# Performance work log

Hardware: AMD Instinct MI355X
Metric: run time of the kernel (lower is better)

The kernel has to match this reference:

```python
import jax, jax.numpy as jnp
import numpy as np

N_AGENTS, OBS_DIM, HID, ACT_DIM = 8192, 64, 128, 16


def setup_inputs() -> dict:
    key = jax.random.key(0)
    k = jax.random.split(key, 8)
    obs_agents = jax.random.normal(k[0], (N_AGENTS, OBS_DIM), dtype=jnp.float32)
    # binary adjacency, {0,1}, int32 (index/mask semantics, non-differentiable)
    adj = jax.random.randint(k[1], (N_AGENTS, N_AGENTS), 0, 2, dtype=jnp.int32)
    def lin(kk, fan_in, fan_out):
        lim = 1.0 / np.sqrt(fan_in)
        kw, kb = jax.random.split(kk)
        W = jax.random.uniform(kw, (fan_in, fan_out), jnp.float32, -lim, lim)
        b = jax.random.uniform(kb, (fan_out,), jnp.float32, -lim, lim)
        return W, b
    W1, b1 = lin(k[2], OBS_DIM, HID)          # encoder
    W2, b2 = lin(k[3], 2 * HID, HID)          # actor layer 1
    W3, b3 = lin(k[4], HID, ACT_DIM)          # actor layer 2
    return {"obs_agents": obs_agents, "adj": adj,
            "W1": W1, "b1": b1, "W2": W2, "b2": b2, "W3": W3, "b3": b3}


def reference(obs_agents, adj, W1, b1, W2, b2, W3, b3):
    # per-agent encode: h = tanh(obs @ W1 + b1)  -> [N, HID]
    h = jnp.tanh(obs_agents @ W1 + b1)
    # neighbor mean message: mean of h[j] over j with adj[i,j]!=0, zeros if no neighbors
    a = adj.astype(h.dtype)                      # [N, N] binary
    deg = jnp.sum(a, axis=1, keepdims=True)      # [N, 1]
    msg = (a @ h) / jnp.maximum(deg, 1.0)        # zero rows stay zero
    # actor MLP on concat([h, msg])
    combined = jnp.concatenate([h, msg], axis=-1)            # [N, 2*HID]
    hid = jnp.tanh(combined @ W2 + b2)                        # [N, HID]
    logits = hid @ W3 + b3                                    # [N, ACT_DIM]
    return logits
```

## Files before the change

kernel.cpp:

```cpp
#include <hip/hip_runtime.h>
#include <stdint.h>
#include <math.h>

#define NAG 8192
#define NB  144
#define BM  64
#define BK  32
#define NSPLIT 8

typedef __attribute__((ext_vector_type(8))) short short8;
typedef __attribute__((ext_vector_type(4))) float floatx4;

__device__ __forceinline__ float bf2f(unsigned short u) {
    union { uint32_t i; float f; } v; v.i = ((uint32_t)u) << 16; return v.f;
}
__device__ __forceinline__ unsigned short f2bf(float f) {
    union { float f; uint32_t i; } v; v.f = f;
    uint32_t x = v.i;
    return (unsigned short)((x + 0x7FFFu + ((x >> 16) & 1u)) >> 16);
}
__device__ __forceinline__ unsigned short f2h(float f) {
    union { _Float16 h; unsigned short u; } v; v.h = (_Float16)f; return v.u;
}
__device__ __forceinline__ float h2f(unsigned short u) {
    union { _Float16 h; unsigned short u; } v; v.u = u; return (float)v.h;
}
__device__ __forceinline__ void gload_lds16(const void* g, void* lds) {
    __builtin_amdgcn_global_load_lds(
        (const __attribute__((address_space(1))) uint32_t*)g,
        (__attribute__((address_space(3))) uint32_t*)lds, 16, 0, 0);
}

__global__ __launch_bounds__(64) void k0_init(
    int* __restrict__ flag, const unsigned short* __restrict__ W1raw)
{
    int big = 0;
    #pragma unroll
    for (int j = 0; j < 8; ++j) {
        float v = bf2f(W1raw[threadIdx.x * 8 + j]);
        if (!(fabsf(v) <= 1e6f)) big = 1;
    }
    unsigned long long m = __ballot(big);
    if (threadIdx.x == 0) *flag = (m != 0ull) ? 1 : 0;
}

__global__ __launch_bounds__(256) void k1_encode(
    const void* __restrict__ obs,
    const void* __restrict__ W1,
    const void* __restrict__ b1,
    const int* __restrict__ flag,
    float* __restrict__ h_f32,
    unsigned short* __restrict__ hT)
{
    __shared__ float obs_lds[32][68];
    __shared__ unsigned short ht_lds[128][33];
    const int t = threadIdx.x;
    const int abase = blockIdx.x * 32;
    const bool isf = (*flag != 0);

    {
        int a = t >> 3, c0 = (t & 7) * 8;
        if (isf) {
            const float* p = (const float*)obs;
            #pragma unroll
            for (int j = 0; j < 8; ++j)
                obs_lds[a][c0 + j] = p[(size_t)(abase + a) * 64 + c0 + j];
        } else {
            const unsigned short* p = (const unsigned short*)obs;
            #pragma unroll
            for (int j = 0; j < 8; ++j)
                obs_lds[a][c0 + j] = bf2f(p[(size_t)(abase + a) * 64 + c0 + j]);
        }
    }
    __syncthreads();

    const int o = t & 127;
    const int half = t >> 7;
    float acc[16];
    if (isf) {
        const float* Wp = (const float*)W1;
        float bias = ((const float*)b1)[o];
        #pragma unroll
        for (int i = 0; i < 16; ++i) acc[i] = bias;
        for (int k0 = 0; k0 < 64; k0 += 8) {
            float w[8];
            #pragma unroll
            for (int j = 0; j < 8; ++j) w[j] = Wp[(k0 + j) * 128 + o];
            #pragma unroll
            for (int j = 0; j < 8; ++j)
                #pragma unroll
                for (int i = 0; i < 16; ++i)
                    acc[i] = fmaf(obs_lds[half * 16 + i][k0 + j], w[j], acc[i]);
        }
    } else {
        const unsigned short* Wp = (const unsigned short*)W1;
        float bias = bf2f(((const unsigned short*)b1)[o]);
        #pragma unroll
        for (int i = 0; i < 16; ++i) acc[i] = bias;
        for (int k0 = 0; k0 < 64; k0 += 8) {
            float w[8];
            #pragma unroll
            for (int j = 0; j < 8; ++j) w[j] = bf2f(Wp[(k0 + j) * 128 + o]);
            #pragma unroll
            for (int j = 0; j < 8; ++j)
                #pragma unroll
                for (int i = 0; i < 16; ++i)
                    acc[i] = fmaf(obs_lds[half * 16 + i][k0 + j], w[j], acc[i]);
        }
    }
    #pragma unroll
    for (int i = 0; i < 16; ++i) {
        float th = tanhf(acc[i]);
        int a = half * 16 + i;
        h_f32[(size_t)(abase + a) * 128 + o] = th;
        ht_lds[o][a] = f2bf(th);
    }
    __syncthreads();

    for (int p = 0; p < 18; ++p) {
        int n = p * 8 + (t >> 5);
        int a = t & 31;
        unsigned short v;
        if (n < 128)       v = ht_lds[n][a];
        else if (n == 128) v = 0x3F80;
        else               v = 0;
        hT[(size_t)n * NAG + abase + a] = v;
    }
}

__global__ __launch_bounds__(256, 4) void k2_msggemm(
    const int* __restrict__ adj,
    const unsigned short* __restrict__ hT,
    unsigned short* __restrict__ Cp16)
{
    __shared__ __align__(16) int Alds0[64 * BK];
    __shared__ __align__(16) int Alds1[64 * BK];
    __shared__ __align__(16) unsigned short Blds0[144 * BK];
    __shared__ __align__(16) unsigned short Blds1[144 * BK];
    const int t = threadIdx.x;
    const int mtile = blockIdx.x & 127;
    const int ks = blockIdx.x >> 7;
    const int row0 = mtile * BM;
    const int kbeg = ks * 1024;

    const int wave = t >> 6, lane = t & 63;
    const int fm = lane & 15, quad = lane >> 4;

    floatx4 acc[9];
    #pragma unroll
    for (int i = 0; i < 9; ++i) acc[i] = (floatx4)0.f;

    const int rowA = wave * 8 + (lane >> 3);
    const int cA = (lane & 7) ^ (rowA & 7);
    const int* aS0 = adj + (size_t)(row0 + rowA) * NAG + kbeg + cA * 4;
    const int* aS1 = adj + (size_t)(row0 + rowA + 32) * NAG + kbeg + cA * 4;
    const int rowB = wave * 16 + (lane >> 2);
    const int cB = (lane & 3) ^ ((rowB >> 1) & 3);
    const unsigned short* bS0 = hT + (size_t)rowB * NAG + kbeg + cB * 8;
    const unsigned short* bS1 = hT + (size_t)(rowB + 64) * NAG + kbeg + cB * 8;
    int* Ad00 = Alds0 + wave * 256;  int* Ad01 = Alds0 + 1024 + wave * 256;
    int* Ad10 = Alds1 + wave * 256;  int* Ad11 = Alds1 + 1024 + wave * 256;
    unsigned short* Bd00 = Blds0 + wave * 512;  unsigned short* Bd01 = Blds0 + 2048 + wave * 512;
    unsigned short* Bd10 = Blds1 + wave * 512;  unsigned short* Bd11 = Blds1 + 2048 + wave * 512;

    {
        int rr = 128 + (t >> 4);
        int off = (t & 15) * 2;
        uint32_t vv = (rr == 128) ? 0x3F803F80u : 0u;
        *reinterpret_cast<uint32_t*>(&Blds0[rr * BK + off]) = vv;
        *reinterpret_cast<uint32_t*>(&Blds1[rr * BK + off]) = vv;
    }

#define DMA(T, Ad0_, Ad1_, Bd0_, Bd1_) do { \
        gload_lds16(aS0 + (T) * BK, (Ad0_)); \
        gload_lds16(aS1 + (T) * BK, (Ad1_)); \
        gload_lds16(bS0 + (T) * BK, (Bd0_)); \
        gload_lds16(bS1 + (T) * BK, (Bd1_)); \
    } while (0)
#define COMPUTE(Ab, Bb) do { \
        const int arow = (wave * 16 + fm) * BK; \
        int4 v0 = *reinterpret_cast<const int4*>(&(Ab)[arow + (((quad * 2 + 0) ^ (fm & 7)) << 2)]); \
        int4 v1 = *reinterpret_cast<const int4*>(&(Ab)[arow + (((quad * 2 + 1) ^ (fm & 7)) << 2)]); \
        union { uint32_t u[4]; short8 s; } af; \
        af.u[0] = ((uint32_t)v0.x | ((uint32_t)v0.y << 16)) * 0x3F80u; \
        af.u[1] = ((uint32_t)v0.z | ((uint32_t)v0.w << 16)) * 0x3F80u; \
        af.u[2] = ((uint32_t)v1.x | ((uint32_t)v1.y << 16)) * 0x3F80u; \
        af.u[3] = ((uint32_t)v1.z | ((uint32_t)v1.w << 16)) * 0x3F80u; \
        const int bphys = (quad ^ ((fm >> 1) & 3)) << 3; \
        _Pragma("unroll") \
        for (int j = 0; j < 9; ++j) { \
            short8 bf = *reinterpret_cast<const short8*>(&(Bb)[(j * 16 + fm) * BK + bphys]); \
            acc[j] = __builtin_amdgcn_mfma_f32_16x16x32_bf16(af.s, bf, acc[j], 0, 0, 0); \
        } \
    } while (0)

    DMA(0, Ad00, Ad01, Bd00, Bd01);

    for (int it = 0; it < 32; it += 2) {
        __syncthreads();
        DMA(it + 1, Ad10, Ad11, Bd10, Bd11);
        COMPUTE(Alds0, Blds0);
        __syncthreads();
        if (it + 2 < 32) DMA(it + 2, Ad00, Ad01, Bd00, Bd01);
        COMPUTE(Alds1, Blds1);
    }

    unsigned short* out = Cp16 + (size_t)ks * (NAG * NB);
    #pragma unroll
    for (int j = 0; j < 9; ++j) {
        int col = j * 16 + fm;
        #pragma unroll
        for (int r = 0; r < 4; ++r) {
            int row = row0 + wave * 16 + quad * 4 + r;
            out[(size_t)row * NB + col] = f2h(acc[j][r]);
        }
    }
#undef DMA
#undef COMPUTE
}

__global__ __launch_bounds__(256) void k3_actor(
    const float* __restrict__ h_f32,
    const unsigned short* __restrict__ Cp16,
    const void* __restrict__ W2,
    const void* __restrict__ b2,
    const void* __restrict__ W3,
    const void* __restrict__ b3,
    const int* __restrict__ flag,
    void* __restrict__ out)
{
    __shared__ float4 comb4[16][66];
    __shared__ float hid[16][132];
    __shared__ float inv_lds[16];
    const int t = threadIdx.x;
    const int abase = blockIdx.x * 16;
    const bool isf = (*flag != 0);
    const size_t PS = (size_t)NAG * NB;

    if (t < 16) {
        float deg = 0.f;
        #pragma unroll
        for (int s = 0; s < NSPLIT; ++s)
            deg += h2f(Cp16[s * PS + (size_t)(abase + t) * NB + 128]);
        inv_lds[t] = 1.0f / fmaxf(deg, 1.0f);
    }
    __syncthreads();

    #pragma unroll
    for (int jj = 0; jj < 4; ++jj) {
        int idx = jj * 256 + t;
        int a = idx >> 6, q = idx & 63;
        float4 v;
        if (q < 32) {
            v = *reinterpret_cast<const float4*>(h_f32 + (size_t)(abase + a) * 128 + q * 4);
        } else {
            int f = (q - 32) * 4;
            float s0 = 0.f, s1 = 0.f, s2 = 0.f, s3 = 0.f;
            #pragma unroll
            for (int s = 0; s < NSPLIT; ++s) {
                ushort4 p = *reinterpret_cast<const ushort4*>(Cp16 + s * PS + (size_t)(abase + a) * NB + f);
                s0 += h2f(p.x); s1 += h2f(p.y); s2 += h2f(p.z); s3 += h2f(p.w);
            }
            float sc = inv_lds[a];
            v = make_float4(s0 * sc, s1 * sc, s2 * sc, s3 * sc);
        }
        comb4[a][q] = v;
    }
    __syncthreads();

    const int o = t & 127, half = t >> 7;
    float acc[8];
    if (isf) {
        const float* Wp = (const float*)W2;
        float bias = ((const float*)b2)[o];
        #pragma unroll
        for (int i = 0; i < 8; ++i) acc[i] = bias;
        for (int cq = 0; cq < 64; ++cq) {
            float w0 = Wp[(cq * 4 + 0) * 128 + o];
            float w1 = Wp[(cq * 4 + 1) * 128 + o];
            float w2 = Wp[(cq * 4 + 2) * 128 + o];
            float w3 = Wp[(cq * 4 + 3) * 128 + o];
            #pragma unroll
            for (int i = 0; i < 8; ++i) {
                float4 v = comb4[half * 8 + i][cq];
                acc[i] = fmaf(v.x, w0, acc[i]);
                acc[i] = fmaf(v.y, w1, acc[i]);
                acc[i] = fmaf(v.z, w2, acc[i]);
                acc[i] = fmaf(v.w, w3, acc[i]);
            }
        }
    } else {
        const unsigned short* Wp = (const unsigned short*)W2;
        float bias = bf2f(((const unsigned short*)b2)[o]);
        #pragma unroll
        for (int i = 0; i < 8; ++i) acc[i] = bias;
        for (int cq = 0; cq < 64; ++cq) {
            float w0 = bf2f(Wp[(cq * 4 + 0) * 128 + o]);
            float w1 = bf2f(Wp[(cq * 4 + 1) * 128 + o]);
            float w2 = bf2f(Wp[(cq * 4 + 2) * 128 + o]);
            float w3 = bf2f(Wp[(cq * 4 + 3) * 128 + o]);
            #pragma unroll
            for (int i = 0; i < 8; ++i) {
                float4 v = comb4[half * 8 + i][cq];
                acc[i] = fmaf(v.x, w0, acc[i]);
                acc[i] = fmaf(v.y, w1, acc[i]);
                acc[i] = fmaf(v.z, w2, acc[i]);
                acc[i] = fmaf(v.w, w3, acc[i]);
            }
        }
    }
    #pragma unroll
    for (int i = 0; i < 8; ++i)
        hid[half * 8 + i][o] = tanhf(acc[i]);
    __syncthreads();

    const int q = t & 15, ar = t >> 4;
    float l;
    if (isf) {
        const float* Wp = (const float*)W3;
        l = ((const float*)b3)[q];
        #pragma unroll 4
        for (int oo = 0; oo < 128; ++oo)
            l = fmaf(hid[ar][oo], Wp[oo * 16 + q], l);
    } else {
        const unsigned short* Wp = (const unsigned short*)W3;
        l = bf2f(((const unsigned short*)b3)[q]);
        #pragma unroll 4
        for (int oo = 0; oo < 128; ++oo)
            l = fmaf(hid[ar][oo], bf2f(Wp[oo * 16 + q]), l);
    }
    size_t i0 = (size_t)(abase + ar) * 16 + q;
    if (isf) ((float*)out)[i0] = l;
    else     ((unsigned short*)out)[i0] = f2bf(l);
}

extern "C" void kernel_launch(void* const* d_in, const int* in_sizes, int n_in,
                              void* d_out, int out_size, void* d_ws, size_t ws_size,
                              hipStream_t stream) {
    const void* obs = d_in[0];
    const int*  adj = (const int*)d_in[1];
    const void* W1  = d_in[2];
    const void* b1  = d_in[3];
    const void* W2  = d_in[4];
    const void* b2  = d_in[5];
    const void* W3  = d_in[6];
    const void* b3  = d_in[7];

    char* ws = (char*)d_ws;
    unsigned short* hT   = (unsigned short*)(ws);
    float*          h_f32= (float*)(ws + 2359296);
    unsigned short* Cp16 = (unsigned short*)(ws + 6553600);
    int*            flag = (int*)(ws + 25427968);

    hipLaunchKernelGGL(k0_init, dim3(1), dim3(64), 0, stream, flag, (const unsigned short*)W1);
    hipLaunchKernelGGL(k1_encode, dim3(256), dim3(256), 0, stream, obs, W1, b1, flag, h_f32, hT);
    hipLaunchKernelGGL(k2_msggemm, dim3(1024), dim3(256), 0, stream, adj, hT, Cp16);
    hipLaunchKernelGGL(k3_actor, dim3(512), dim3(256), 0, stream, h_f32, Cp16, W2, b2, W3, b3, flag, d_out);
}
```

Baseline: 469.7 us.

## Load adjacency directly into registers and double split-K for message GEMM

```diff
diff --git a/kernel.cpp b/kernel.cpp
--- a/kernel.cpp
+++ b/kernel.cpp
@@ -6,7 +6,7 @@
 #define NB  144
 #define BM  64
 #define BK  32
-#define NSPLIT 8
+#define NSPLIT 16
 
 typedef __attribute__((ext_vector_type(8))) short short8;
 typedef __attribute__((ext_vector_type(4))) float floatx4;
@@ -133,15 +133,13 @@
     const unsigned short* __restrict__ hT,
     unsigned short* __restrict__ Cp16)
 {
-    __shared__ __align__(16) int Alds0[64 * BK];
-    __shared__ __align__(16) int Alds1[64 * BK];
     __shared__ __align__(16) unsigned short Blds0[144 * BK];
     __shared__ __align__(16) unsigned short Blds1[144 * BK];
     const int t = threadIdx.x;
     const int mtile = blockIdx.x & 127;
     const int ks = blockIdx.x >> 7;
     const int row0 = mtile * BM;
-    const int kbeg = ks * 1024;
+    const int kbeg = ks * 512;
 
     const int wave = t >> 6, lane = t & 63;
     const int fm = lane & 15, quad = lane >> 4;
@@ -150,16 +148,12 @@
     #pragma unroll
     for (int i = 0; i < 9; ++i) acc[i] = (floatx4)0.f;
 
-    const int rowA = wave * 8 + (lane >> 3);
-    const int cA = (lane & 7) ^ (rowA & 7);
-    const int* aS0 = adj + (size_t)(row0 + rowA) * NAG + kbeg + cA * 4;
-    const int* aS1 = adj + (size_t)(row0 + rowA + 32) * NAG + kbeg + cA * 4;
+    const int* aP = adj + (size_t)(row0 + wave * 16 + fm) * NAG + kbeg + quad * 8;
+
     const int rowB = wave * 16 + (lane >> 2);
     const int cB = (lane & 3) ^ ((rowB >> 1) & 3);
     const unsigned short* bS0 = hT + (size_t)rowB * NAG + kbeg + cB * 8;
     const unsigned short* bS1 = hT + (size_t)(rowB + 64) * NAG + kbeg + cB * 8;
-    int* Ad00 = Alds0 + wave * 256;  int* Ad01 = Alds0 + 1024 + wave * 256;
-    int* Ad10 = Alds1 + wave * 256;  int* Ad11 = Alds1 + 1024 + wave * 256;
     unsigned short* Bd00 = Blds0 + wave * 512;  unsigned short* Bd01 = Blds0 + 2048 + wave * 512;
     unsigned short* Bd10 = Blds1 + wave * 512;  unsigned short* Bd11 = Blds1 + 2048 + wave * 512;
 
@@ -171,16 +165,13 @@
         *reinterpret_cast<uint32_t*>(&Blds1[rr * BK + off]) = vv;
     }
 
-#define DMA(T, Ad0_, Ad1_, Bd0_, Bd1_) do { \
-        gload_lds16(aS0 + (T) * BK, (Ad0_)); \
-        gload_lds16(aS1 + (T) * BK, (Ad1_)); \
+#define DMAB(T, Bd0_, Bd1_) do { \
         gload_lds16(bS0 + (T) * BK, (Bd0_)); \
         gload_lds16(bS1 + (T) * BK, (Bd1_)); \
     } while (0)
-#define COMPUTE(Ab, Bb) do { \
-        const int arow = (wave * 16 + fm) * BK; \
-        int4 v0 = *reinterpret_cast<const int4*>(&(Ab)[arow + (((quad * 2 + 0) ^ (fm & 7)) << 2)]); \
-        int4 v1 = *reinterpret_cast<const int4*>(&(Ab)[arow + (((quad * 2 + 1) ^ (fm & 7)) << 2)]); \
+#define COMPUTE(T, Bb) do { \
+        int4 v0 = *reinterpret_cast<const int4*>(aP + (T) * BK); \
+        int4 v1 = *reinterpret_cast<const int4*>(aP + (T) * BK + 4); \
         union { uint32_t u[4]; short8 s; } af; \
         af.u[0] = ((uint32_t)v0.x | ((uint32_t)v0.y << 16)) * 0x3F80u; \
         af.u[1] = ((uint32_t)v0.z | ((uint32_t)v0.w << 16)) * 0x3F80u; \
@@ -194,15 +185,15 @@
         } \
     } while (0)
 
-    DMA(0, Ad00, Ad01, Bd00, Bd01);
-
-    for (int it = 0; it < 32; it += 2) {
+    DMAB(0, Bd00, Bd01);
+
+    for (int it = 0; it < 16; it += 2) {
         __syncthreads();
-        DMA(it + 1, Ad10, Ad11, Bd10, Bd11);
-        COMPUTE(Alds0, Blds0);
+        DMAB(it + 1, Bd10, Bd11);
+        COMPUTE(it, Blds0);
         __syncthreads();
-        if (it + 2 < 32) DMA(it + 2, Ad00, Ad01, Bd00, Bd01);
-        COMPUTE(Alds1, Blds1);
+        if (it + 2 < 16) DMAB(it + 2, Bd00, Bd01);
+        COMPUTE(it + 1, Blds1);
     }
 
     unsigned short* out = Cp16 + (size_t)ks * (NAG * NB);
@@ -215,7 +206,7 @@
             out[(size_t)row * NB + col] = f2h(acc[j][r]);
         }
     }
-#undef DMA
+#undef DMAB
 #undef COMPUTE
 }
 
@@ -350,10 +341,10 @@
     unsigned short* hT   = (unsigned short*)(ws);
     float*          h_f32= (float*)(ws + 2359296);
     unsigned short* Cp16 = (unsigned short*)(ws + 6553600);
-    int*            flag = (int*)(ws + 25427968);
+    int*            flag = (int*)(ws + 44302336);
 
     hipLaunchKernelGGL(k0_init, dim3(1), dim3(64), 0, stream, flag, (const unsigned short*)W1);
     hipLaunchKernelGGL(k1_encode, dim3(256), dim3(256), 0, stream, obs, W1, b1, flag, h_f32, hT);
-    hipLaunchKernelGGL(k2_msggemm, dim3(1024), dim3(256), 0, stream, adj, hT, Cp16);
+    hipLaunchKernelGGL(k2_msggemm, dim3(2048), dim3(256), 0, stream, adj, hT, Cp16);
     hipLaunchKernelGGL(k3_actor, dim3(512), dim3(256), 0, stream, h_f32, Cp16, W2, b2, W3, b3, flag, d_out);
 }
```

Result: faster. 460.3 us (-2.0%).
